# Kernel optimization log

Hardware: AMD Instinct MI355X
Metric: run time of the kernel (lower is better)

## Reference

```python
import jax, jax.numpy as jnp
import numpy as np

S, B, IN, H, OUT = 512, 64, 512, 1024, 512


def _glorot(key, shape, fan_in):
    bound = 1.0 / np.sqrt(fan_in)
    return jax.random.uniform(key, shape, jnp.float32, -bound, bound)


def setup_inputs() -> dict:
    key = jax.random.key(0)
    ks = jax.random.split(key, 16)
    inp = {"x": jax.random.normal(ks[0], (S, B, IN), jnp.float32)}
    # layer 0: input IN -> H ; layer 1: H -> H. Gates stacked [f,i,o,c] -> 4H rows.
    inp["l0_Wx"] = _glorot(ks[1], (4 * H, IN), IN)
    inp["l0_Uh"] = _glorot(ks[2], (4 * H, H), H)
    inp["l0_bx"] = _glorot(ks[3], (4 * H,), IN)
    inp["l0_bh"] = _glorot(ks[4], (4 * H,), H)
    inp["l1_Wx"] = _glorot(ks[5], (4 * H, H), H)
    inp["l1_Uh"] = _glorot(ks[6], (4 * H, H), H)
    inp["l1_bx"] = _glorot(ks[7], (4 * H,), H)
    inp["l1_bh"] = _glorot(ks[8], (4 * H,), H)
    inp["fc_W"] = _glorot(ks[9], (OUT, H), H)
    inp["fc_b"] = _glorot(ks[10], (OUT,), H)
    return inp


def lstm_layer(x, Wx, Uh, bx, bh):
    # Precompute input projections for all timesteps in one big GEMM
    # (same math as per-step input2{f,i,o,c} Linears).
    xp = jnp.einsum("sbi,gi->sbg", x, Wx) + bx  # [S,B,4H]
    h0 = jnp.zeros((x.shape[1], H), x.dtype)
    c0 = jnp.zeros((x.shape[1], H), x.dtype)

    def step(carry, xp_t):
        h, c = carry
        gates = xp_t + h @ Uh.T + bh  # [B,4H]
        f, i, o, g = jnp.split(gates, 4, axis=-1)
        f, i, o = jax.nn.sigmoid(f), jax.nn.sigmoid(i), jax.nn.sigmoid(o)
        c = f * c + i * jnp.tanh(g)
        h = o * jnp.tanh(c)
        return (h, c), h

    (_, _), outs = jax.lax.scan(step, (h0, c0), xp)
    return outs  # [S,B,H]


def reference(x, l0_Wx, l0_Uh, l0_bx, l0_bh, l1_Wx, l1_Uh, l1_bx, l1_bh, fc_W, fc_b):
    h = lstm_layer(x, l0_Wx, l0_Uh, l0_bx, l0_bh)
    # hidden_activation_function defaults to Identity between layers
    h = lstm_layer(h, l1_Wx, l1_Uh, l1_bx, l1_bh)
    out = jnp.einsum("sbh,oh->sbo", h, fc_W) + fc_b  # [S,B,OUT]
    return out
```

## Files before the change

### kernel.cpp

```cpp
#include <hip/hip_runtime.h>
#include <hip/hip_bf16.h>

#define SDIM 512
#define BDIM 64
#define INDIM 512
#define HDIM 1024
#define OUTDIM 512
#define NWG 256
#define THREADS 512
#define BH (BDIM * HDIM)

typedef __bf16 bfreg;
typedef bfreg bf16x8 __attribute__((ext_vector_type(8)));
typedef bfreg bf16x4 __attribute__((ext_vector_type(4)));
typedef float f32x4 __attribute__((ext_vector_type(4)));

__device__ __forceinline__ float sigf(float x) { return 1.f / (1.f + __expf(-x)); }
__device__ __forceinline__ float tanhfast(float x) { return 1.f - 2.f / (__expf(2.f * x) + 1.f); }


__global__ void cvt_bf16(bfreg* __restrict__ dst, const float* __restrict__ src, int n4)
{
    for (int i = blockIdx.x * blockDim.x + threadIdx.x; i < n4; i += gridDim.x * blockDim.x) {
        const float4 v = *(const float4*)(src + (size_t)i * 4);
        bf16x4 o;
        o[0] = (bfreg)v.x; o[1] = (bfreg)v.y; o[2] = (bfreg)v.z; o[3] = (bfreg)v.w;
        *(bf16x4*)(dst + (size_t)i * 4) = o;
    }
}

__global__ void bias_combine(float* __restrict__ b0, const float* __restrict__ bx0,
                             const float* __restrict__ bh0,
                             float* __restrict__ b1, const float* __restrict__ bx1,
                             const float* __restrict__ bh1)
{
    int i = blockIdx.x * blockDim.x + threadIdx.x;
    if (i < 4 * HDIM) {
        b0[i] = bx0[i] + bh0[i];
        b1[i] = bx1[i] + bh1[i];
    }
}

__global__ void pack_x(bfreg* __restrict__ dst, const float* __restrict__ src)
{
    const int total = SDIM * (INDIM / 8) * BDIM;
    for (int idx = blockIdx.x * blockDim.x + threadIdx.x; idx < total;
         idx += gridDim.x * blockDim.x) {
        const int b = idx & (BDIM - 1);
        const int r = idx >> 6;
        const int kb = r & (INDIM / 8 - 1);
        const int t = r >> 6;
        const float* s = src + ((size_t)t * BDIM + b) * INDIM + kb * 8;
        bfreg* d = dst + (size_t)idx * 8;
        #pragma unroll
        for (int j = 0; j < 8; ++j) d[j] = (bfreg)s[j];
    }
}

__global__ void pack_w(bfreg* __restrict__ dst, const float* __restrict__ Wx,
                       const float* __restrict__ Uh, int K0, int KH)
{
    const int KST = (K0 + KH) / 32;
    const int total = 128 * 2 * KST * 64;
    for (int idx = blockIdx.x * blockDim.x + threadIdx.x; idx < total;
         idx += gridDim.x * blockDim.x) {
        const int lane = idx & 63;
        int rem = idx >> 6;
        const int ks = rem % KST; rem /= KST;
        const int nt = rem & 1;
        const int wg = rem >> 1;
        const int rr = nt * 16 + (lane & 15);
        const int g = rr >> 3, uo = rr & 7;
        const int row = g * HDIM + wg * 8 + uo;
        const int k = ks * 32 + (lane >> 4) * 8;
        const float* s = (k < K0) ? Wx + (size_t)row * K0 + k
                                  : Uh + (size_t)row * KH + (k - K0);
        bfreg* d = dst + (size_t)idx * 8;
        #pragma unroll
        for (int j = 0; j < 8; ++j) d[j] = (bfreg)s[j];
    }
}


__device__ __forceinline__ void wait_gen(const unsigned* g)
{
    while (__hip_atomic_load(g, __ATOMIC_RELAXED, __HIP_MEMORY_SCOPE_AGENT) == 0u)
        __builtin_amdgcn_s_sleep(1);
}

__device__ __forceinline__ void lds_spin(int* r, int target)
{
    while (__hip_atomic_load(r, __ATOMIC_ACQUIRE, __HIP_MEMORY_SCOPE_WORKGROUP) < target)
        __builtin_amdgcn_s_sleep(1);
}

template<int LAYER>
__device__ __forceinline__ void scan_layer(
    const bfreg* __restrict__ Pw, const float* __restrict__ biasL,
    const bfreg* __restrict__ x_pk,
    bfreg* __restrict__ Hb0, bfreg* __restrict__ Hb1,
    unsigned* __restrict__ sub0, unsigned* __restrict__ sub1,
    unsigned* __restrict__ gen0, unsigned* __restrict__ gen1,
    const int rg, char* smem)
{
    constexpr int KST = LAYER ? 64 : 48;
    constexpr int ECNT = LAYER ? 16 : 8;
    constexpr int LCNT = 16;

    const int tid = threadIdx.x;
    const int l = tid & 63;
    const int wid = tid >> 6;
    const int m = wid & 3;
    const int kh = wid >> 2;

    bfreg* lW = (bfreg*)smem;
    float* gatebuf = (float*)(smem + 64 * 2048);
    float* cbuf = gatebuf + 2 * 32 * 68;
    float* lbias = cbuf + 8 * 68;
    int* ready = (int*)(lbias + 32);

    {
        const float4* wsrc = (const float4*)(Pw + (size_t)rg * ((size_t)KST * 1024));
        float4* wdst = (float4*)lW;
        for (int i = tid; i < KST * 128; i += THREADS) wdst[i] = wsrc[i];
    }
    if (tid < 32) lbias[tid] = biasL[(tid >> 3) * HDIM + rg * 8 + (tid & 7)];
    if (tid < 3) ready[tid] = 0;
    for (int i = tid; i < 8 * 68; i += THREADS) cbuf[i] = 0.f;
    __syncthreads();

    const int cl = l & 15, kg = l >> 4;
    const int rowA = m * 16 + cl;
    const int e_beg = LAYER ? (32 + kh * 16) : (kh * 8);
    const int l_beg = LAYER ? (kh * 16) : (16 + kh * 16);

    unsigned* mysub = LAYER ? sub1 : sub0;
    unsigned* mygen = LAYER ? gen1 : gen0;
    bfreg* Hme = LAYER ? Hb1 : Hb0;
    int* done = ready + 2;

    for (int t = 0; t < SDIM; ++t) {
        f32x4 acc0 = {0.f, 0.f, 0.f, 0.f};
        f32x4 acc1 = {0.f, 0.f, 0.f, 0.f};
        bf16x8 ev[ECNT];
        bf16x8 av[LCNT];

        if (!LAYER) {
            const bfreg* s0 = x_pk + (size_t)t * (64 * BDIM * 8);
            #pragma unroll
            for (int i = 0; i < ECNT; ++i) {
                const int cb = (e_beg + i) * 4 + kg;
                ev[i] = *(const bf16x8*)(s0 + (size_t)cb * 512 + rowA * 8);
            }
            __builtin_amdgcn_sched_barrier(0);
            if (t > 0) {
                if (wid == 0) {
                    wait_gen(gen0 + (size_t)(t - 1) * 16);
                    __hip_atomic_store(&ready[0], t, __ATOMIC_RELEASE,
                                       __HIP_MEMORY_SCOPE_WORKGROUP);
                } else {
                    lds_spin(&ready[0], t);
                }
            }
            asm volatile("" ::: "memory");
            const bfreg* s1 = Hb0 + (size_t)t * BH;
            #pragma unroll
            for (int i = 0; i < LCNT; ++i) {
                const int cb = (l_beg + i) * 4 + kg - 64;
                av[i] = *(const bf16x8*)(s1 + (size_t)cb * 512 + rowA * 8);
            }
            __builtin_amdgcn_sched_barrier(0);
        } else {
            if (wid == 0) {
                wait_gen(gen0 + (size_t)t * 16);
                __hip_atomic_store(&ready[0], t + 1, __ATOMIC_RELEASE,
                                   __HIP_MEMORY_SCOPE_WORKGROUP);
            } else {
                lds_spin(&ready[0], t + 1);
            }
            asm volatile("" ::: "memory");
            const bfreg* s0 = Hb0 + (size_t)(t + 1) * BH;
            #pragma unroll
            for (int i = 0; i < LCNT; ++i) {
                const int cb = (l_beg + i) * 4 + kg;
                av[i] = *(const bf16x8*)(s0 + (size_t)cb * 512 + rowA * 8);
            }
            __builtin_amdgcn_sched_barrier(0);
            if (t > 0) {
                if (wid == 4) {
                    wait_gen(gen1 + (size_t)(t - 1) * 16);
                    __hip_atomic_store(&ready[1], t, __ATOMIC_RELEASE,
                                       __HIP_MEMORY_SCOPE_WORKGROUP);
                } else {
                    lds_spin(&ready[1], t);
                }
            }
            asm volatile("" ::: "memory");
            const bfreg* s1 = Hb1 + (size_t)t * BH;
            #pragma unroll
            for (int i = 0; i < ECNT; ++i) {
                const int cb = (e_beg + i) * 4 + kg - 128;
                ev[i] = *(const bf16x8*)(s1 + (size_t)cb * 512 + rowA * 8);
            }
            __builtin_amdgcn_sched_barrier(0);
        }

        if (!LAYER) {
            #pragma unroll
            for (int i = 0; i < ECNT; ++i) {
                const int ks = e_beg + i;
                const bf16x8 w0 = *(const bf16x8*)(lW + ((size_t)ks * 64 + l) * 8);
                const bf16x8 w1 = *(const bf16x8*)(lW + ((size_t)(KST + ks) * 64 + l) * 8);
                acc0 = __builtin_amdgcn_mfma_f32_16x16x32_bf16(ev[i], w0, acc0, 0, 0, 0);
                acc1 = __builtin_amdgcn_mfma_f32_16x16x32_bf16(ev[i], w1, acc1, 0, 0, 0);
            }
            #pragma unroll
            for (int i = 0; i < LCNT; ++i) {
                const int ks = l_beg + i;
                const bf16x8 w0 = *(const bf16x8*)(lW + ((size_t)ks * 64 + l) * 8);
                const bf16x8 w1 = *(const bf16x8*)(lW + ((size_t)(KST + ks) * 64 + l) * 8);
                acc0 = __builtin_amdgcn_mfma_f32_16x16x32_bf16(av[i], w0, acc0, 0, 0, 0);
                acc1 = __builtin_amdgcn_mfma_f32_16x16x32_bf16(av[i], w1, acc1, 0, 0, 0);
            }
        } else {
            #pragma unroll
            for (int i = 0; i < LCNT; ++i) {
                const int ks = l_beg + i;
                const bf16x8 w0 = *(const bf16x8*)(lW + ((size_t)ks * 64 + l) * 8);
                const bf16x8 w1 = *(const bf16x8*)(lW + ((size_t)(KST + ks) * 64 + l) * 8);
                acc0 = __builtin_amdgcn_mfma_f32_16x16x32_bf16(av[i], w0, acc0, 0, 0, 0);
                acc1 = __builtin_amdgcn_mfma_f32_16x16x32_bf16(av[i], w1, acc1, 0, 0, 0);
            }
            #pragma unroll
            for (int i = 0; i < ECNT; ++i) {
                const int ks = e_beg + i;
                const bf16x8 w0 = *(const bf16x8*)(lW + ((size_t)ks * 64 + l) * 8);
                const bf16x8 w1 = *(const bf16x8*)(lW + ((size_t)(KST + ks) * 64 + l) * 8);
                acc0 = __builtin_amdgcn_mfma_f32_16x16x32_bf16(ev[i], w0, acc0, 0, 0, 0);
                acc1 = __builtin_amdgcn_mfma_f32_16x16x32_bf16(ev[i], w1, acc1, 0, 0, 0);
            }
        }

        float* gb = gatebuf + kh * (32 * 68);
        const int bb = m * 16 + (l >> 4) * 4;
        *(f32x4*)(gb + (0 * 16 + cl) * 68 + bb) = acc0;
        *(f32x4*)(gb + (1 * 16 + cl) * 68 + bb) = acc1;
        __syncthreads();

        {
            const int uo = tid & 7, b = tid >> 3;
            float* g0 = gatebuf;
            float* g1 = gatebuf + 32 * 68;
            const float fv = g0[uo * 68 + b]        + g1[uo * 68 + b]        + lbias[uo];
            const float iv = g0[(8 + uo) * 68 + b]  + g1[(8 + uo) * 68 + b]  + lbias[8 + uo];
            const float ov = g0[(16 + uo) * 68 + b] + g1[(16 + uo) * 68 + b] + lbias[16 + uo];
            const float gv = g0[(24 + uo) * 68 + b] + g1[(24 + uo) * 68 + b] + lbias[24 + uo];
            const float c = cbuf[uo * 68 + b];
            const float fg = sigf(fv), ig = sigf(iv), og = sigf(ov);
            const float gg = tanhfast(gv);
            const float cn = fg * c + ig * gg;
            cbuf[uo * 68 + b] = cn;
            const bfreg hv = (bfreg)(og * tanhfast(cn));
            unsigned short hs;
            __builtin_memcpy(&hs, &hv, 2);
            const unsigned hw = hs;
            bfreg* dp = Hme + (size_t)(t + 1) * BH + rg * 512 + tid;
            asm volatile("global_store_short %0, %1, off sc0 sc1"
                         :: "v"(dp), "v"(hw) : "memory");
            asm volatile("s_waitcnt vmcnt(0)" ::: "memory");
        }
        if (l == 0)
            __hip_atomic_fetch_add(done, 1, __ATOMIC_ACQ_REL,
                                   __HIP_MEMORY_SCOPE_WORKGROUP);
        if (wid == 1) {
            while (__hip_atomic_load(done, __ATOMIC_ACQUIRE,
                                     __HIP_MEMORY_SCOPE_WORKGROUP) < 8 * (t + 1))
                __builtin_amdgcn_s_sleep(1);
            if (l == 0)
                __hip_atomic_fetch_add(mysub + (size_t)t * 128 + (rg >> 4) * 16, 1u,
                                       __ATOMIC_RELAXED, __HIP_MEMORY_SCOPE_AGENT);
        }
        if (rg == 0 && wid == 2) {
            const unsigned* sc = mysub + (size_t)t * 128;
            while (true) {
                unsigned v = (l < 8)
                    ? __hip_atomic_load(sc + l * 16, __ATOMIC_RELAXED,
                                        __HIP_MEMORY_SCOPE_AGENT)
                    : 16u;
                if (__all(v >= 16u)) break;
                __builtin_amdgcn_s_sleep(1);
            }
            asm volatile("" ::: "memory");
            if (l == 0)
                __hip_atomic_store(mygen + (size_t)t * 16, 1u,
                                   __ATOMIC_RELEASE, __HIP_MEMORY_SCOPE_AGENT);
        }
    }
}

__global__ __launch_bounds__(THREADS, 2)
void lstm_scan(const bfreg* __restrict__ Pw0, const bfreg* __restrict__ Pw1,
               const float* __restrict__ bias0, const float* __restrict__ bias1,
               const bfreg* __restrict__ x_pk,
               bfreg* __restrict__ Hb0, bfreg* __restrict__ Hb1,
               unsigned* __restrict__ sub0, unsigned* __restrict__ sub1,
               unsigned* __restrict__ gen0, unsigned* __restrict__ gen1)
{
    extern __shared__ char smem[];
    const int wgid = blockIdx.x;
    const int rg = wgid >> 1;
    if (wgid & 1)
        scan_layer<1>(Pw1, bias1, x_pk, Hb0, Hb1, sub0, sub1, gen0, gen1, rg, smem);
    else
        scan_layer<0>(Pw0, bias0, x_pk, Hb0, Hb1, sub0, sub1, gen0, gen1, rg, smem);
}

__global__ void fc_gemm(const bfreg* __restrict__ Hb1, const bfreg* __restrict__ Wb,
                        const float* __restrict__ bias, float* __restrict__ out)
{
    const int lane = threadIdx.x & 63;
    const int wid = threadIdx.x >> 6;
    const int cl = lane & 15, kg = lane >> 4;
    const int mbase = blockIdx.y * 64 + (wid >> 1) * 32;
    const int nbase = blockIdx.x * 64 + (wid & 1) * 32;
    const int t = mbase >> 6;
    const int b0 = mbase & 63;
    const bfreg* pa0 = Hb1 + (size_t)(t + 1) * BH + (size_t)kg * 512 + (b0 + cl) * 8;
    const bfreg* pa1 = pa0 + 16 * 8;
    const bfreg* pb0 = Wb + (size_t)(nbase + cl) * HDIM + kg * 8;
    const bfreg* pb1 = pb0 + (size_t)16 * HDIM;
    f32x4 acc[2][2] = {};
    #pragma unroll 4
    for (int k = 0; k < HDIM; k += 32) {
        const size_t co = (size_t)(k >> 3) * 512;
        const bf16x8 av0 = *(const bf16x8*)(pa0 + co);
        const bf16x8 av1 = *(const bf16x8*)(pa1 + co);
        const bf16x8 bv0 = *(const bf16x8*)(pb0 + k);
        const bf16x8 bv1 = *(const bf16x8*)(pb1 + k);
        acc[0][0] = __builtin_amdgcn_mfma_f32_16x16x32_bf16(av0, bv0, acc[0][0], 0, 0, 0);
        acc[0][1] = __builtin_amdgcn_mfma_f32_16x16x32_bf16(av0, bv1, acc[0][1], 0, 0, 0);
        acc[1][0] = __builtin_amdgcn_mfma_f32_16x16x32_bf16(av1, bv0, acc[1][0], 0, 0, 0);
        acc[1][1] = __builtin_amdgcn_mfma_f32_16x16x32_bf16(av1, bv1, acc[1][1], 0, 0, 0);
    }
    #pragma unroll
    for (int mi = 0; mi < 2; ++mi)
        #pragma unroll
        for (int ni = 0; ni < 2; ++ni)
            #pragma unroll
            for (int r = 0; r < 4; ++r) {
                const int row = mbase + mi * 16 + kg * 4 + r;
                const int col = nbase + ni * 16 + cl;
                out[(size_t)row * OUTDIM + col] = acc[mi][ni][r] + bias[col];
            }
}

extern "C" void kernel_launch(void* const* d_in, const int* in_sizes, int n_in,
                              void* d_out, int out_size, void* d_ws, size_t ws_size,
                              hipStream_t stream)
{
    const float* x     = (const float*)d_in[0];
    const float* l0_Wx = (const float*)d_in[1];
    const float* l0_Uh = (const float*)d_in[2];
    const float* l0_bx = (const float*)d_in[3];
    const float* l0_bh = (const float*)d_in[4];
    const float* l1_Wx = (const float*)d_in[5];
    const float* l1_Uh = (const float*)d_in[6];
    const float* l1_bx = (const float*)d_in[7];
    const float* l1_bh = (const float*)d_in[8];
    const float* fc_W  = (const float*)d_in[9];
    const float* fc_b  = (const float*)d_in[10];
    (void)in_sizes; (void)n_in; (void)out_size; (void)ws_size;

    char* p = (char*)d_ws;
    size_t off = 0;
    auto take = [&](size_t bytes) {
        void* r = p + off;
        off = (off + bytes + 255) & ~(size_t)255;
        return r;
    };

    bfreg* x_pk  = (bfreg*)take((size_t)SDIM * BDIM * INDIM * 2);
    bfreg* Pw0   = (bfreg*)take((size_t)128 * 48 * 1024 * 2);
    bfreg* Pw1   = (bfreg*)take((size_t)128 * 64 * 1024 * 2);
    bfreg* fcWb  = (bfreg*)take((size_t)OUTDIM * HDIM * 2);
    float* bias0 = (float*)take((size_t)4 * HDIM * 4);
    float* bias1 = (float*)take((size_t)4 * HDIM * 4);
    bfreg* Hb0   = (bfreg*)take((size_t)(SDIM + 1) * BH * 2);
    bfreg* Hb1   = (bfreg*)take((size_t)(SDIM + 1) * BH * 2);
    unsigned* sub0 = (unsigned*)take((size_t)SDIM * 128 * 4);
    unsigned* sub1 = (unsigned*)take((size_t)SDIM * 128 * 4);
    unsigned* gen0 = (unsigned*)take((size_t)SDIM * 16 * 4);
    unsigned* gen1 = (unsigned*)take((size_t)SDIM * 16 * 4);

    hipMemsetAsync(Hb0, 0, (size_t)BH * 2, stream);
    hipMemsetAsync(Hb1, 0, (size_t)BH * 2, stream);
    hipMemsetAsync(sub0, 0, (size_t)SDIM * 128 * 4, stream);
    hipMemsetAsync(sub1, 0, (size_t)SDIM * 128 * 4, stream);
    hipMemsetAsync(gen0, 0, (size_t)SDIM * 16 * 4, stream);
    hipMemsetAsync(gen1, 0, (size_t)SDIM * 16 * 4, stream);

    pack_x<<<4096, 256, 0, stream>>>(x_pk, x);
    cvt_bf16<<<512, 256, 0, stream>>>(fcWb, fc_W, OUTDIM * HDIM / 4);
    pack_w<<<3072, 256, 0, stream>>>(Pw0, l0_Wx, l0_Uh, INDIM, HDIM);
    pack_w<<<4096, 256, 0, stream>>>(Pw1, l1_Wx, l1_Uh, HDIM, HDIM);
    bias_combine<<<16, 256, 0, stream>>>(bias0, l0_bx, l0_bh, bias1, l1_bx, l1_bh);

    const int smem_bytes = 64 * 2048 + 2 * 32 * 68 * 4 + 8 * 68 * 4 + 32 * 4 + 16;
    hipFuncSetAttribute((const void*)lstm_scan,
                        hipFuncAttributeMaxDynamicSharedMemorySize, smem_bytes);
    lstm_scan<<<NWG, THREADS, smem_bytes, stream>>>(Pw0, Pw1, bias0, bias1,
                                                    x_pk, Hb0, Hb1,
                                                    sub0, sub1, gen0, gen1);

    fc_gemm<<<dim3(OUTDIM / 64, SDIM * BDIM / 64), 256, 0, stream>>>(
        Hb1, fcWb, fc_b, (float*)d_out);
}
```

Measured before the change: 2.779 ms.

## Replace polling master barrier with last-arriver tree counter and reorder step loads

```diff
diff --git a/kernel.cpp b/kernel.cpp
--- a/kernel.cpp
+++ b/kernel.cpp
@@ -100,6 +100,7 @@
     const bfreg* __restrict__ x_pk,
     bfreg* __restrict__ Hb0, bfreg* __restrict__ Hb1,
     unsigned* __restrict__ sub0, unsigned* __restrict__ sub1,
+    unsigned* __restrict__ lvl0, unsigned* __restrict__ lvl1,
     unsigned* __restrict__ gen0, unsigned* __restrict__ gen1,
     const int rg, char* smem)
 {
@@ -135,6 +136,7 @@
     const int l_beg = LAYER ? (kh * 16) : (16 + kh * 16);
 
     unsigned* mysub = LAYER ? sub1 : sub0;
+    unsigned* mylvl = LAYER ? lvl1 : lvl0;
     unsigned* mygen = LAYER ? gen1 : gen0;
     bfreg* Hme = LAYER ? Hb1 : Hb0;
     int* done = ready + 2;
@@ -153,6 +155,36 @@
                 ev[i] = *(const bf16x8*)(s0 + (size_t)cb * 512 + rowA * 8);
             }
             __builtin_amdgcn_sched_barrier(0);
+        } else {
+            if (t > 0) {
+                if (wid == 4) {
+                    wait_gen(gen1 + (size_t)(t - 1) * 16);
+                    __hip_atomic_store(&ready[1], t, __ATOMIC_RELEASE,
+                                       __HIP_MEMORY_SCOPE_WORKGROUP);
+                } else {
+                    lds_spin(&ready[1], t);
+                }
+            }
+            asm volatile("" ::: "memory");
+            const bfreg* s1 = Hb1 + (size_t)t * BH;
+            #pragma unroll
+            for (int i = 0; i < ECNT; ++i) {
+                const int cb = (e_beg + i) * 4 + kg - 128;
+                ev[i] = *(const bf16x8*)(s1 + (size_t)cb * 512 + rowA * 8);
+            }
+            __builtin_amdgcn_sched_barrier(0);
+        }
+        #pragma unroll
+        for (int i = 0; i < ECNT; ++i) {
+            const int ks = e_beg + i;
+            const bf16x8 w0 = *(const bf16x8*)(lW + ((size_t)ks * 64 + l) * 8);
+            const bf16x8 w1 = *(const bf16x8*)(lW + ((size_t)(KST + ks) * 64 + l) * 8);
+            acc0 = __builtin_amdgcn_mfma_f32_16x16x32_bf16(ev[i], w0, acc0, 0, 0, 0);
+            acc1 = __builtin_amdgcn_mfma_f32_16x16x32_bf16(ev[i], w1, acc1, 0, 0, 0);
+        }
+        __builtin_amdgcn_sched_barrier(0);
+
+        if (!LAYER) {
             if (t > 0) {
                 if (wid == 0) {
                     wait_gen(gen0 + (size_t)(t - 1) * 16);
@@ -162,14 +194,6 @@
                     lds_spin(&ready[0], t);
                 }
             }
-            asm volatile("" ::: "memory");
-            const bfreg* s1 = Hb0 + (size_t)t * BH;
-            #pragma unroll
-            for (int i = 0; i < LCNT; ++i) {
-                const int cb = (l_beg + i) * 4 + kg - 64;
-                av[i] = *(const bf16x8*)(s1 + (size_t)cb * 512 + rowA * 8);
-            }
-            __builtin_amdgcn_sched_barrier(0);
         } else {
             if (wid == 0) {
                 wait_gen(gen0 + (size_t)t * 16);
@@ -178,42 +202,18 @@
             } else {
                 lds_spin(&ready[0], t + 1);
             }
-            asm volatile("" ::: "memory");
-            const bfreg* s0 = Hb0 + (size_t)(t + 1) * BH;
+        }
+        asm volatile("" ::: "memory");
+
+        {
+            const bfreg* sl = LAYER ? (Hb0 + (size_t)(t + 1) * BH)
+                                    : (Hb0 + (size_t)t * BH);
             #pragma unroll
             for (int i = 0; i < LCNT; ++i) {
-                const int cb = (l_beg + i) * 4 + kg;
-                av[i] = *(const bf16x8*)(s0 + (size_t)cb * 512 + rowA * 8);
+                const int cb = (l_beg + i) * 4 + kg - (LAYER ? 0 : 64);
+                av[i] = *(const bf16x8*)(sl + (size_t)cb * 512 + rowA * 8);
             }
             __builtin_amdgcn_sched_barrier(0);
-            if (t > 0) {
-                if (wid == 4) {
-                    wait_gen(gen1 + (size_t)(t - 1) * 16);
-                    __hip_atomic_store(&ready[1], t, __ATOMIC_RELEASE,
-                                       __HIP_MEMORY_SCOPE_WORKGROUP);
-                } else {
-                    lds_spin(&ready[1], t);
-                }
-            }
-            asm volatile("" ::: "memory");
-            const bfreg* s1 = Hb1 + (size_t)t * BH;
-            #pragma unroll
-            for (int i = 0; i < ECNT; ++i) {
-                const int cb = (e_beg + i) * 4 + kg - 128;
-                ev[i] = *(const bf16x8*)(s1 + (size_t)cb * 512 + rowA * 8);
-            }
-            __builtin_amdgcn_sched_barrier(0);
-        }
-
-        if (!LAYER) {
-            #pragma unroll
-            for (int i = 0; i < ECNT; ++i) {
-                const int ks = e_beg + i;
-                const bf16x8 w0 = *(const bf16x8*)(lW + ((size_t)ks * 64 + l) * 8);
-                const bf16x8 w1 = *(const bf16x8*)(lW + ((size_t)(KST + ks) * 64 + l) * 8);
-                acc0 = __builtin_amdgcn_mfma_f32_16x16x32_bf16(ev[i], w0, acc0, 0, 0, 0);
-                acc1 = __builtin_amdgcn_mfma_f32_16x16x32_bf16(ev[i], w1, acc1, 0, 0, 0);
-            }
             #pragma unroll
             for (int i = 0; i < LCNT; ++i) {
                 const int ks = l_beg + i;
@@ -221,23 +221,6 @@
                 const bf16x8 w1 = *(const bf16x8*)(lW + ((size_t)(KST + ks) * 64 + l) * 8);
                 acc0 = __builtin_amdgcn_mfma_f32_16x16x32_bf16(av[i], w0, acc0, 0, 0, 0);
                 acc1 = __builtin_amdgcn_mfma_f32_16x16x32_bf16(av[i], w1, acc1, 0, 0, 0);
-            }
-        } else {
-            #pragma unroll
-            for (int i = 0; i < LCNT; ++i) {
-                const int ks = l_beg + i;
-                const bf16x8 w0 = *(const bf16x8*)(lW + ((size_t)ks * 64 + l) * 8);
-                const bf16x8 w1 = *(const bf16x8*)(lW + ((size_t)(KST + ks) * 64 + l) * 8);
-                acc0 = __builtin_amdgcn_mfma_f32_16x16x32_bf16(av[i], w0, acc0, 0, 0, 0);
-                acc1 = __builtin_amdgcn_mfma_f32_16x16x32_bf16(av[i], w1, acc1, 0, 0, 0);
-            }
-            #pragma unroll
-            for (int i = 0; i < ECNT; ++i) {
-                const int ks = e_beg + i;
-                const bf16x8 w0 = *(const bf16x8*)(lW + ((size_t)ks * 64 + l) * 8);
-                const bf16x8 w1 = *(const bf16x8*)(lW + ((size_t)(KST + ks) * 64 + l) * 8);
-                acc0 = __builtin_amdgcn_mfma_f32_16x16x32_bf16(ev[i], w0, acc0, 0, 0, 0);
-                acc1 = __builtin_amdgcn_mfma_f32_16x16x32_bf16(ev[i], w1, acc1, 0, 0, 0);
             }
         }
 
@@ -276,24 +259,19 @@
             while (__hip_atomic_load(done, __ATOMIC_ACQUIRE,
                                      __HIP_MEMORY_SCOPE_WORKGROUP) < 8 * (t + 1))
                 __builtin_amdgcn_s_sleep(1);
-            if (l == 0)
-                __hip_atomic_fetch_add(mysub + (size_t)t * 128 + (rg >> 4) * 16, 1u,
-                                       __ATOMIC_RELAXED, __HIP_MEMORY_SCOPE_AGENT);
-        }
-        if (rg == 0 && wid == 2) {
-            const unsigned* sc = mysub + (size_t)t * 128;
-            while (true) {
-                unsigned v = (l < 8)
-                    ? __hip_atomic_load(sc + l * 16, __ATOMIC_RELAXED,
-                                        __HIP_MEMORY_SCOPE_AGENT)
-                    : 16u;
-                if (__all(v >= 16u)) break;
-                __builtin_amdgcn_s_sleep(1);
-            }
-            asm volatile("" ::: "memory");
-            if (l == 0)
-                __hip_atomic_store(mygen + (size_t)t * 16, 1u,
-                                   __ATOMIC_RELEASE, __HIP_MEMORY_SCOPE_AGENT);
+            if (l == 0) {
+                unsigned old = __hip_atomic_fetch_add(
+                    mysub + (size_t)t * 128 + (rg >> 4) * 16, 1u,
+                    __ATOMIC_RELAXED, __HIP_MEMORY_SCOPE_AGENT);
+                if (old == 15u) {
+                    unsigned o2 = __hip_atomic_fetch_add(
+                        mylvl + (size_t)t * 16, 1u,
+                        __ATOMIC_RELAXED, __HIP_MEMORY_SCOPE_AGENT);
+                    if (o2 == 7u)
+                        __hip_atomic_store(mygen + (size_t)t * 16, 1u,
+                                           __ATOMIC_RELEASE, __HIP_MEMORY_SCOPE_AGENT);
+                }
+            }
         }
     }
 }
@@ -304,15 +282,18 @@
                const bfreg* __restrict__ x_pk,
                bfreg* __restrict__ Hb0, bfreg* __restrict__ Hb1,
                unsigned* __restrict__ sub0, unsigned* __restrict__ sub1,
+               unsigned* __restrict__ lvl0, unsigned* __restrict__ lvl1,
                unsigned* __restrict__ gen0, unsigned* __restrict__ gen1)
 {
     extern __shared__ char smem[];
     const int wgid = blockIdx.x;
     const int rg = wgid >> 1;
     if (wgid & 1)
-        scan_layer<1>(Pw1, bias1, x_pk, Hb0, Hb1, sub0, sub1, gen0, gen1, rg, smem);
+        scan_layer<1>(Pw1, bias1, x_pk, Hb0, Hb1, sub0, sub1, lvl0, lvl1,
+                      gen0, gen1, rg, smem);
     else
-        scan_layer<0>(Pw0, bias0, x_pk, Hb0, Hb1, sub0, sub1, gen0, gen1, rg, smem);
+        scan_layer<0>(Pw0, bias0, x_pk, Hb0, Hb1, sub0, sub1, lvl0, lvl1,
+                      gen0, gen1, rg, smem);
 }
 
 __global__ void fc_gemm(const bfreg* __restrict__ Hb1, const bfreg* __restrict__ Wb,
@@ -389,6 +370,8 @@
     bfreg* Hb1   = (bfreg*)take((size_t)(SDIM + 1) * BH * 2);
     unsigned* sub0 = (unsigned*)take((size_t)SDIM * 128 * 4);
     unsigned* sub1 = (unsigned*)take((size_t)SDIM * 128 * 4);
+    unsigned* lvl0 = (unsigned*)take((size_t)SDIM * 16 * 4);
+    unsigned* lvl1 = (unsigned*)take((size_t)SDIM * 16 * 4);
     unsigned* gen0 = (unsigned*)take((size_t)SDIM * 16 * 4);
     unsigned* gen1 = (unsigned*)take((size_t)SDIM * 16 * 4);
 
@@ -396,6 +379,8 @@
     hipMemsetAsync(Hb1, 0, (size_t)BH * 2, stream);
     hipMemsetAsync(sub0, 0, (size_t)SDIM * 128 * 4, stream);
     hipMemsetAsync(sub1, 0, (size_t)SDIM * 128 * 4, stream);
+    hipMemsetAsync(lvl0, 0, (size_t)SDIM * 16 * 4, stream);
+    hipMemsetAsync(lvl1, 0, (size_t)SDIM * 16 * 4, stream);
     hipMemsetAsync(gen0, 0, (size_t)SDIM * 16 * 4, stream);
     hipMemsetAsync(gen1, 0, (size_t)SDIM * 16 * 4, stream);
 
@@ -410,7 +395,8 @@
                         hipFuncAttributeMaxDynamicSharedMemorySize, smem_bytes);
     lstm_scan<<<NWG, THREADS, smem_bytes, stream>>>(Pw0, Pw1, bias0, bias1,
                                                     x_pk, Hb0, Hb1,
-                                                    sub0, sub1, gen0, gen1);
+                                                    sub0, sub1, lvl0, lvl1,
+                                                    gen0, gen1);
 
     fc_gemm<<<dim3(OUTDIM / 64, SDIM * BDIM / 64), 256, 0, stream>>>(
         Hb1, fcWb, fc_b, (float*)d_out);
```

Result: slower. 2.906 ms (+4.6%).

## Switch recurrent gate GEMM to 32x32x16 MFMA with four-way K split

Applied to the files above, without the earlier changes.

```diff
diff --git a/kernel.cpp b/kernel.cpp
--- a/kernel.cpp
+++ b/kernel.cpp
@@ -14,6 +14,7 @@
 typedef bfreg bf16x8 __attribute__((ext_vector_type(8)));
 typedef bfreg bf16x4 __attribute__((ext_vector_type(4)));
 typedef float f32x4 __attribute__((ext_vector_type(4)));
+typedef float f32x16 __attribute__((ext_vector_type(16)));
 
 __device__ __forceinline__ float sigf(float x) { return 1.f / (1.f + __expf(-x)); }
 __device__ __forceinline__ float tanhfast(float x) { return 1.f - 2.f / (__expf(2.f * x) + 1.f); }
@@ -60,19 +61,18 @@
 __global__ void pack_w(bfreg* __restrict__ dst, const float* __restrict__ Wx,
                        const float* __restrict__ Uh, int K0, int KH)
 {
-    const int KST = (K0 + KH) / 32;
-    const int total = 128 * 2 * KST * 64;
+    const int KST16 = (K0 + KH) / 16;
+    const int total = 128 * KST16 * 64;
     for (int idx = blockIdx.x * blockDim.x + threadIdx.x; idx < total;
          idx += gridDim.x * blockDim.x) {
         const int lane = idx & 63;
         int rem = idx >> 6;
-        const int ks = rem % KST; rem /= KST;
-        const int nt = rem & 1;
-        const int wg = rem >> 1;
-        const int rr = nt * 16 + (lane & 15);
+        const int ks = rem % KST16;
+        const int wg = rem / KST16;
+        const int rr = lane & 31;
         const int g = rr >> 3, uo = rr & 7;
         const int row = g * HDIM + wg * 8 + uo;
-        const int k = ks * 32 + (lane >> 4) * 8;
+        const int k = ks * 16 + (lane >> 5) * 8;
         const float* s = (k < K0) ? Wx + (size_t)row * K0 + k
                                   : Uh + (size_t)row * KH + (k - K0);
         bfreg* d = dst + (size_t)idx * 8;
@@ -103,36 +103,36 @@
     unsigned* __restrict__ gen0, unsigned* __restrict__ gen1,
     const int rg, char* smem)
 {
-    constexpr int KST = LAYER ? 64 : 48;
+    constexpr int KST16 = LAYER ? 128 : 96;
     constexpr int ECNT = LAYER ? 16 : 8;
     constexpr int LCNT = 16;
 
     const int tid = threadIdx.x;
     const int l = tid & 63;
     const int wid = tid >> 6;
-    const int m = wid & 3;
-    const int kh = wid >> 2;
+    const int m = wid & 1;
+    const int kq = wid >> 1;
 
     bfreg* lW = (bfreg*)smem;
-    float* gatebuf = (float*)(smem + 64 * 2048);
+    float* gatebuf = (float*)(smem + 128 * 1024);
     float* cbuf = gatebuf + 2 * 32 * 68;
     float* lbias = cbuf + 8 * 68;
     int* ready = (int*)(lbias + 32);
 
     {
-        const float4* wsrc = (const float4*)(Pw + (size_t)rg * ((size_t)KST * 1024));
+        const float4* wsrc = (const float4*)(Pw + (size_t)rg * ((size_t)KST16 * 512));
         float4* wdst = (float4*)lW;
-        for (int i = tid; i < KST * 128; i += THREADS) wdst[i] = wsrc[i];
+        for (int i = tid; i < KST16 * 64; i += THREADS) wdst[i] = wsrc[i];
     }
     if (tid < 32) lbias[tid] = biasL[(tid >> 3) * HDIM + rg * 8 + (tid & 7)];
     if (tid < 3) ready[tid] = 0;
     for (int i = tid; i < 8 * 68; i += THREADS) cbuf[i] = 0.f;
     __syncthreads();
 
-    const int cl = l & 15, kg = l >> 4;
-    const int rowA = m * 16 + cl;
-    const int e_beg = LAYER ? (32 + kh * 16) : (kh * 8);
-    const int l_beg = LAYER ? (kh * 16) : (16 + kh * 16);
+    const int rowA = m * 32 + (l & 31);
+    const int k8 = l >> 5;
+    const int rr = l & 31;
+    const int boff = 4 * (l >> 5);
 
     unsigned* mysub = LAYER ? sub1 : sub0;
     unsigned* mygen = LAYER ? gen1 : gen0;
@@ -140,8 +140,7 @@
     int* done = ready + 2;
 
     for (int t = 0; t < SDIM; ++t) {
-        f32x4 acc0 = {0.f, 0.f, 0.f, 0.f};
-        f32x4 acc1 = {0.f, 0.f, 0.f, 0.f};
+        f32x16 acc = {};
         bf16x8 ev[ECNT];
         bf16x8 av[LCNT];
 
@@ -149,7 +148,8 @@
             const bfreg* s0 = x_pk + (size_t)t * (64 * BDIM * 8);
             #pragma unroll
             for (int i = 0; i < ECNT; ++i) {
-                const int cb = (e_beg + i) * 4 + kg;
+                const int ks = kq + 4 * i;
+                const int cb = ks * 2 + k8;
                 ev[i] = *(const bf16x8*)(s0 + (size_t)cb * 512 + rowA * 8);
             }
             __builtin_amdgcn_sched_barrier(0);
@@ -166,7 +166,8 @@
             const bfreg* s1 = Hb0 + (size_t)t * BH;
             #pragma unroll
             for (int i = 0; i < LCNT; ++i) {
-                const int cb = (l_beg + i) * 4 + kg - 64;
+                const int ks = kq + 4 * (8 + i);
+                const int cb = (ks - 32) * 2 + k8;
                 av[i] = *(const bf16x8*)(s1 + (size_t)cb * 512 + rowA * 8);
             }
             __builtin_amdgcn_sched_barrier(0);
@@ -182,7 +183,8 @@
             const bfreg* s0 = Hb0 + (size_t)(t + 1) * BH;
             #pragma unroll
             for (int i = 0; i < LCNT; ++i) {
-                const int cb = (l_beg + i) * 4 + kg;
+                const int ks = kq + 4 * i;
+                const int cb = ks * 2 + k8;
                 av[i] = *(const bf16x8*)(s0 + (size_t)cb * 512 + rowA * 8);
             }
             __builtin_amdgcn_sched_barrier(0);
@@ -199,7 +201,8 @@
             const bfreg* s1 = Hb1 + (size_t)t * BH;
             #pragma unroll
             for (int i = 0; i < ECNT; ++i) {
-                const int cb = (e_beg + i) * 4 + kg - 128;
+                const int ks = kq + 4 * (16 + i);
+                const int cb = (ks - 64) * 2 + k8;
                 ev[i] = *(const bf16x8*)(s1 + (size_t)cb * 512 + rowA * 8);
             }
             __builtin_amdgcn_sched_barrier(0);
@@ -208,43 +211,51 @@
         if (!LAYER) {
             #pragma unroll
             for (int i = 0; i < ECNT; ++i) {
-                const int ks = e_beg + i;
-                const bf16x8 w0 = *(const bf16x8*)(lW + ((size_t)ks * 64 + l) * 8);
-                const bf16x8 w1 = *(const bf16x8*)(lW + ((size_t)(KST + ks) * 64 + l) * 8);
-                acc0 = __builtin_amdgcn_mfma_f32_16x16x32_bf16(ev[i], w0, acc0, 0, 0, 0);
-                acc1 = __builtin_amdgcn_mfma_f32_16x16x32_bf16(ev[i], w1, acc1, 0, 0, 0);
+                const int ks = kq + 4 * i;
+                const bf16x8 w = *(const bf16x8*)(lW + ((size_t)ks * 64 + l) * 8);
+                acc = __builtin_amdgcn_mfma_f32_32x32x16_bf16(ev[i], w, acc, 0, 0, 0);
             }
             #pragma unroll
             for (int i = 0; i < LCNT; ++i) {
-                const int ks = l_beg + i;
-                const bf16x8 w0 = *(const bf16x8*)(lW + ((size_t)ks * 64 + l) * 8);
-                const bf16x8 w1 = *(const bf16x8*)(lW + ((size_t)(KST + ks) * 64 + l) * 8);
-                acc0 = __builtin_amdgcn_mfma_f32_16x16x32_bf16(av[i], w0, acc0, 0, 0, 0);
-                acc1 = __builtin_amdgcn_mfma_f32_16x16x32_bf16(av[i], w1, acc1, 0, 0, 0);
+                const int ks = kq + 4 * (8 + i);
+                const bf16x8 w = *(const bf16x8*)(lW + ((size_t)ks * 64 + l) * 8);
+                acc = __builtin_amdgcn_mfma_f32_32x32x16_bf16(av[i], w, acc, 0, 0, 0);
             }
         } else {
             #pragma unroll
             for (int i = 0; i < LCNT; ++i) {
-                const int ks = l_beg + i;
-                const bf16x8 w0 = *(const bf16x8*)(lW + ((size_t)ks * 64 + l) * 8);
-                const bf16x8 w1 = *(const bf16x8*)(lW + ((size_t)(KST + ks) * 64 + l) * 8);
-                acc0 = __builtin_amdgcn_mfma_f32_16x16x32_bf16(av[i], w0, acc0, 0, 0, 0);
-                acc1 = __builtin_amdgcn_mfma_f32_16x16x32_bf16(av[i], w1, acc1, 0, 0, 0);
+                const int ks = kq + 4 * i;
+                const bf16x8 w = *(const bf16x8*)(lW + ((size_t)ks * 64 + l) * 8);
+                acc = __builtin_amdgcn_mfma_f32_32x32x16_bf16(av[i], w, acc, 0, 0, 0);
             }
             #pragma unroll
             for (int i = 0; i < ECNT; ++i) {
-                const int ks = e_beg + i;
-                const bf16x8 w0 = *(const bf16x8*)(lW + ((size_t)ks * 64 + l) * 8);
-                const bf16x8 w1 = *(const bf16x8*)(lW + ((size_t)(KST + ks) * 64 + l) * 8);
-                acc0 = __builtin_amdgcn_mfma_f32_16x16x32_bf16(ev[i], w0, acc0, 0, 0, 0);
-                acc1 = __builtin_amdgcn_mfma_f32_16x16x32_bf16(ev[i], w1, acc1, 0, 0, 0);
-            }
-        }
-
-        float* gb = gatebuf + kh * (32 * 68);
-        const int bb = m * 16 + (l >> 4) * 4;
-        *(f32x4*)(gb + (0 * 16 + cl) * 68 + bb) = acc0;
-        *(f32x4*)(gb + (1 * 16 + cl) * 68 + bb) = acc1;
+                const int ks = kq + 4 * (16 + i);
+                const bf16x8 w = *(const bf16x8*)(lW + ((size_t)ks * 64 + l) * 8);
+                acc = __builtin_amdgcn_mfma_f32_32x32x16_bf16(ev[i], w, acc, 0, 0, 0);
+            }
+        }
+
+        if (wid >= 4) {
+            float* slot = gatebuf + (kq - 2) * (32 * 68);
+            #pragma unroll
+            for (int q = 0; q < 4; ++q) {
+                f32x4 v = { acc[4 * q], acc[4 * q + 1], acc[4 * q + 2], acc[4 * q + 3] };
+                *(f32x4*)(slot + rr * 68 + m * 32 + 8 * q + boff) = v;
+            }
+        }
+        __syncthreads();
+        if (wid < 4) {
+            float* slot = gatebuf + kq * (32 * 68);
+            #pragma unroll
+            for (int q = 0; q < 4; ++q) {
+                float* pp = slot + rr * 68 + m * 32 + 8 * q + boff;
+                f32x4 v = *(f32x4*)pp;
+                v[0] += acc[4 * q];     v[1] += acc[4 * q + 1];
+                v[2] += acc[4 * q + 2]; v[3] += acc[4 * q + 3];
+                *(f32x4*)pp = v;
+            }
+        }
         __syncthreads();
 
         {
@@ -380,8 +391,8 @@
     };
 
     bfreg* x_pk  = (bfreg*)take((size_t)SDIM * BDIM * INDIM * 2);
-    bfreg* Pw0   = (bfreg*)take((size_t)128 * 48 * 1024 * 2);
-    bfreg* Pw1   = (bfreg*)take((size_t)128 * 64 * 1024 * 2);
+    bfreg* Pw0   = (bfreg*)take((size_t)128 * 96 * 512 * 2);
+    bfreg* Pw1   = (bfreg*)take((size_t)128 * 128 * 512 * 2);
     bfreg* fcWb  = (bfreg*)take((size_t)OUTDIM * HDIM * 2);
     float* bias0 = (float*)take((size_t)4 * HDIM * 4);
     float* bias1 = (float*)take((size_t)4 * HDIM * 4);
@@ -405,7 +416,7 @@
     pack_w<<<4096, 256, 0, stream>>>(Pw1, l1_Wx, l1_Uh, HDIM, HDIM);
     bias_combine<<<16, 256, 0, stream>>>(bias0, l0_bx, l0_bh, bias1, l1_bx, l1_bh);
 
-    const int smem_bytes = 64 * 2048 + 2 * 32 * 68 * 4 + 8 * 68 * 4 + 32 * 4 + 16;
+    const int smem_bytes = 128 * 1024 + 2 * 32 * 68 * 4 + 8 * 68 * 4 + 32 * 4 + 16;
     hipFuncSetAttribute((const void*)lstm_scan,
                         hipFuncAttributeMaxDynamicSharedMemorySize, smem_bytes);
     lstm_scan<<<NWG, THREADS, smem_bytes, stream>>>(Pw0, Pw1, bias0, bias1,
```

Measured after the change: 2.726 ms, median of 2. No clear change (-1.9%).
